# Performance work log

Hardware: AMD Instinct MI355X
Metric: run time of the kernel (lower is better)

The kernel has to match this reference:

```python
import jax, jax.numpy as jnp
import numpy as np

N_SRC = 100000
N_DST = 100000
N_EDGES = 1000000
D = 64


def setup_inputs() -> dict:
    key = jax.random.key(0)
    k1, k2, k3 = jax.random.split(key, 3)
    src_emb = jax.random.normal(k1, (N_SRC, D), dtype=jnp.float32)
    edge_src = jax.random.randint(k2, (N_EDGES,), 0, N_SRC, dtype=jnp.int64)
    edge_dst = jax.random.randint(k3, (N_EDGES,), 0, N_DST, dtype=jnp.int64)
    return {"src_emb": src_emb, "edge_src": edge_src, "edge_dst": edge_dst, "num_dst": N_DST}


def reference(src_emb, edge_src, edge_dst, num_dst):
    # copy_u: gather source features onto edges; sum: scatter-add to dst nodes.
    messages = src_emb[edge_src]  # [E, D]
    dst_emb = jax.ops.segment_sum(messages, edge_dst, num_segments=num_dst)  # [N_dst, D]
    return dst_emb
```

## Files before the change

kernel.cpp:

```cpp
#include <hip/hip_runtime.h>


#define DPB 256
#define BIN_SHIFT 8
#define EPB 4096

__device__ __forceinline__ unsigned short f2bf(float f) {
    unsigned u = __float_as_uint(f);
    unsigned r = u + 0x7FFFu + ((u >> 16) & 1u);
    return (unsigned short)(r >> 16);
}
__device__ __forceinline__ unsigned pack2(float lo, float hi) {
    return (unsigned)f2bf(lo) | ((unsigned)f2bf(hi) << 16);
}

__global__ void convert_bf16_kernel(const float4* __restrict__ src4,
                                    uint4* __restrict__ srcb, long n8) {
    long t = (long)blockIdx.x * blockDim.x + threadIdx.x;
    if (t >= n8) return;
    float4 a = src4[t * 2];
    float4 b = src4[t * 2 + 1];
    uint4 o;
    o.x = pack2(a.x, a.y);
    o.y = pack2(a.z, a.w);
    o.z = pack2(b.x, b.y);
    o.w = pack2(b.z, b.w);
    srcb[t] = o;
}

__global__ void bin_hist_kernel(const int* __restrict__ edst,
                                int* __restrict__ binCounts,
                                int nbins, int n) {
    __shared__ int lc[1024];
    int t = threadIdx.x;
    for (int k = t; k < nbins; k += blockDim.x) lc[k] = 0;
    __syncthreads();

    int i0 = blockIdx.x * EPB + t * 8;
    if (i0 + 7 < n) {
        int4 d0 = *reinterpret_cast<const int4*>(edst + i0);
        int4 d1 = *reinterpret_cast<const int4*>(edst + i0 + 4);
        atomicAdd(&lc[d0.x >> BIN_SHIFT], 1);
        atomicAdd(&lc[d0.y >> BIN_SHIFT], 1);
        atomicAdd(&lc[d0.z >> BIN_SHIFT], 1);
        atomicAdd(&lc[d0.w >> BIN_SHIFT], 1);
        atomicAdd(&lc[d1.x >> BIN_SHIFT], 1);
        atomicAdd(&lc[d1.y >> BIN_SHIFT], 1);
        atomicAdd(&lc[d1.z >> BIN_SHIFT], 1);
        atomicAdd(&lc[d1.w >> BIN_SHIFT], 1);
    } else {
        for (int k = 0; k < 8; ++k) {
            int i = i0 + k;
            if (i < n) atomicAdd(&lc[edst[i] >> BIN_SHIFT], 1);
        }
    }
    __syncthreads();
    for (int k = t; k < nbins; k += blockDim.x) {
        int c = lc[k];
        if (c > 0) atomicAdd(&binCounts[k], c);
    }
}

__global__ void bin_scan_kernel(int* __restrict__ binOff,
                                int* __restrict__ cursor,
                                int nbins) {
    __shared__ int lds[1024];
    int t = threadIdx.x;
    int v = (t < nbins) ? binOff[t] : 0;
    lds[t] = v;
    __syncthreads();
    for (int off = 1; off < 1024; off <<= 1) {
        int u = (t >= off) ? lds[t - off] : 0;
        __syncthreads();
        lds[t] += u;
        __syncthreads();
    }
    if (t < nbins) {
        int base = lds[t] - v;
        binOff[t] = base;
        cursor[t] = base;
    }
    if (t == 1023) binOff[nbins] = lds[t];
}

__global__ void bin_scatter_kernel(const int* __restrict__ esrc,
                                   const int* __restrict__ edst,
                                   int* __restrict__ cursor,
                                   int* __restrict__ packed,
                                   int nbins, int n) {
    __shared__ int lc[1024];
    __shared__ int lbase[1024];
    __shared__ int lrank[1024];
    int t = threadIdx.x;
    for (int k = t; k < nbins; k += blockDim.x) { lc[k] = 0; lrank[k] = 0; }
    __syncthreads();

    int i0 = blockIdx.x * EPB + t * 8;
    bool fast = (i0 + 7 < n);

    if (fast) {
        int4 d0 = *reinterpret_cast<const int4*>(edst + i0);
        int4 d1 = *reinterpret_cast<const int4*>(edst + i0 + 4);
        atomicAdd(&lc[d0.x >> BIN_SHIFT], 1);
        atomicAdd(&lc[d0.y >> BIN_SHIFT], 1);
        atomicAdd(&lc[d0.z >> BIN_SHIFT], 1);
        atomicAdd(&lc[d0.w >> BIN_SHIFT], 1);
        atomicAdd(&lc[d1.x >> BIN_SHIFT], 1);
        atomicAdd(&lc[d1.y >> BIN_SHIFT], 1);
        atomicAdd(&lc[d1.z >> BIN_SHIFT], 1);
        atomicAdd(&lc[d1.w >> BIN_SHIFT], 1);
    } else {
        for (int k = 0; k < 8; ++k) {
            int i = i0 + k;
            if (i < n) atomicAdd(&lc[edst[i] >> BIN_SHIFT], 1);
        }
    }
    __syncthreads();

    for (int k = t; k < nbins; k += blockDim.x) {
        int c = lc[k];
        if (c > 0) lbase[k] = atomicAdd(&cursor[k], c);
    }
    __syncthreads();

    if (fast) {
        int4 s0 = *reinterpret_cast<const int4*>(esrc + i0);
        int4 s1 = *reinterpret_cast<const int4*>(esrc + i0 + 4);
        int4 d0 = *reinterpret_cast<const int4*>(edst + i0);
        int4 d1 = *reinterpret_cast<const int4*>(edst + i0 + 4);
        { int k = d0.x >> BIN_SHIFT, r = atomicAdd(&lrank[k], 1);
          packed[lbase[k] + r] = ((d0.x & (DPB - 1)) << 20) | s0.x; }
        { int k = d0.y >> BIN_SHIFT, r = atomicAdd(&lrank[k], 1);
          packed[lbase[k] + r] = ((d0.y & (DPB - 1)) << 20) | s0.y; }
        { int k = d0.z >> BIN_SHIFT, r = atomicAdd(&lrank[k], 1);
          packed[lbase[k] + r] = ((d0.z & (DPB - 1)) << 20) | s0.z; }
        { int k = d0.w >> BIN_SHIFT, r = atomicAdd(&lrank[k], 1);
          packed[lbase[k] + r] = ((d0.w & (DPB - 1)) << 20) | s0.w; }
        { int k = d1.x >> BIN_SHIFT, r = atomicAdd(&lrank[k], 1);
          packed[lbase[k] + r] = ((d1.x & (DPB - 1)) << 20) | s1.x; }
        { int k = d1.y >> BIN_SHIFT, r = atomicAdd(&lrank[k], 1);
          packed[lbase[k] + r] = ((d1.y & (DPB - 1)) << 20) | s1.y; }
        { int k = d1.z >> BIN_SHIFT, r = atomicAdd(&lrank[k], 1);
          packed[lbase[k] + r] = ((d1.z & (DPB - 1)) << 20) | s1.z; }
        { int k = d1.w >> BIN_SHIFT, r = atomicAdd(&lrank[k], 1);
          packed[lbase[k] + r] = ((d1.w & (DPB - 1)) << 20) | s1.w; }
    } else {
        for (int kk = 0; kk < 8; ++kk) {
            int i = i0 + kk;
            if (i < n) {
                int d = edst[i];
                int k = d >> BIN_SHIFT;
                int r = atomicAdd(&lrank[k], 1);
                packed[lbase[k] + r] = ((d & (DPB - 1)) << 20) | esrc[i];
            }
        }
    }
}

__global__ void bin_sort_kernel(const int* __restrict__ packed,
                                const int* __restrict__ binOff,
                                int* __restrict__ sorted_src,
                                int* __restrict__ offsets,
                                int nbins, int n_dst, int n_edges) {
    __shared__ int cnt[DPB];
    __shared__ int base[DPB];
    int t = threadIdx.x;
    int b = blockIdx.x;
    int start = binOff[b];
    int end = binOff[b + 1];

    cnt[t] = 0;
    __syncthreads();
    for (int j = start + t; j < end; j += DPB) {
        atomicAdd(&cnt[(packed[j] >> 20) & (DPB - 1)], 1);
    }
    __syncthreads();
    int v = cnt[t];
    base[t] = v;
    __syncthreads();
    for (int o = 1; o < DPB; o <<= 1) {
        int u = (t >= o) ? base[t - o] : 0;
        __syncthreads();
        base[t] += u;
        __syncthreads();
    }
    int my_excl = base[t] - v;
    __syncthreads();
    base[t] = my_excl;
    cnt[t] = 0;
    int g = (b << BIN_SHIFT) + t;
    if (g < n_dst) offsets[g] = start + my_excl;
    if (b == nbins - 1 && t == 0) offsets[n_dst] = n_edges;
    __syncthreads();
    for (int j = start + t; j < end; j += DPB) {
        int p = packed[j];
        int dl = (p >> 20) & (DPB - 1);
        int r = atomicAdd(&cnt[dl], 1);
        sorted_src[start + base[dl] + r] = p & 0xFFFFF;
    }
}

__global__ void accum_abs_bf16(const uint4* __restrict__ srcb,
                               const int* __restrict__ offsets,
                               const int* __restrict__ sorted_src,
                               float4* __restrict__ out4, int n_dst) {
    int node = blockIdx.x * (blockDim.x >> 6) + (threadIdx.x >> 6);
    if (node >= n_dst) return;
    int lane = threadIdx.x & 63;
    int g = lane >> 3;
    int q = lane & 7;

    int start = offsets[node];
    int end = offsets[node + 1];

    float a0 = 0.f, a1 = 0.f, a2 = 0.f, a3 = 0.f;
    float a4 = 0.f, a5 = 0.f, a6 = 0.f, a7 = 0.f;

    for (int j = start + g; j < end; j += 8) {
        int s = sorted_src[j];
        uint4 v = srcb[(size_t)s * 8 + q];
        a0 += __uint_as_float(v.x << 16);
        a1 += __uint_as_float(v.x & 0xFFFF0000u);
        a2 += __uint_as_float(v.y << 16);
        a3 += __uint_as_float(v.y & 0xFFFF0000u);
        a4 += __uint_as_float(v.z << 16);
        a5 += __uint_as_float(v.z & 0xFFFF0000u);
        a6 += __uint_as_float(v.w << 16);
        a7 += __uint_as_float(v.w & 0xFFFF0000u);
    }

#pragma unroll
    for (int off = 8; off < 64; off <<= 1) {
        a0 += __shfl_xor(a0, off);
        a1 += __shfl_xor(a1, off);
        a2 += __shfl_xor(a2, off);
        a3 += __shfl_xor(a3, off);
        a4 += __shfl_xor(a4, off);
        a5 += __shfl_xor(a5, off);
        a6 += __shfl_xor(a6, off);
        a7 += __shfl_xor(a7, off);
    }
    if (g == 0) {
        size_t o = (size_t)node * 16 + q * 2;
        out4[o]     = make_float4(a0, a1, a2, a3);
        out4[o + 1] = make_float4(a4, a5, a6, a7);
    }
}


__global__ void fused_bucket_convert(const float4* __restrict__ src4,
                                     uint4* __restrict__ srcb, long n8,
                                     const int* __restrict__ esrc,
                                     const int* __restrict__ edst,
                                     int* __restrict__ cnt,
                                     int* __restrict__ bucket, int cap,
                                     int2* __restrict__ spill,
                                     int* __restrict__ spill_cnt, int spill_max,
                                     int n_edges) {
    int i = blockIdx.x * blockDim.x + threadIdx.x;

    int s = 0, r = 0, d = 0;
    bool have_edge = (i < n_edges);
    if (have_edge) {
        d = edst[i];
        s = esrc[i];
        r = atomicAdd(&cnt[d], 1);
    }

    long nthreads = (long)gridDim.x * blockDim.x;
    for (long t = i; t < n8; t += nthreads) {
        float4 a = src4[t * 2];
        float4 b = src4[t * 2 + 1];
        uint4 o;
        o.x = pack2(a.x, a.y);
        o.y = pack2(a.z, a.w);
        o.z = pack2(b.x, b.y);
        o.w = pack2(b.z, b.w);
        srcb[t] = o;
    }

    if (have_edge) {
        if (r < cap) {
            bucket[(size_t)d * cap + r] = s;
        } else {
            int k = atomicAdd(spill_cnt, 1);
            if (k < spill_max) spill[k] = make_int2(s, d);
        }
    }
}

__global__ void accum_bucket_bf16(const uint4* __restrict__ srcb,
                                  const int* __restrict__ cnt,
                                  const int* __restrict__ bucket, int cap,
                                  float4* __restrict__ out4, int n_dst) {
    int node = blockIdx.x * (blockDim.x >> 6) + (threadIdx.x >> 6);
    if (node >= n_dst) return;
    int lane = threadIdx.x & 63;
    int g = lane >> 3;
    int q = lane & 7;

    int cn = cnt[node];
    cn = cn < cap ? cn : cap;
    const int* brow = bucket + (size_t)node * cap;

    float a0 = 0.f, a1 = 0.f, a2 = 0.f, a3 = 0.f;
    float a4 = 0.f, a5 = 0.f, a6 = 0.f, a7 = 0.f;

    for (int j = g; j < cn; j += 8) {
        int s = brow[j];
        uint4 v = srcb[(size_t)s * 8 + q];
        a0 += __uint_as_float(v.x << 16);
        a1 += __uint_as_float(v.x & 0xFFFF0000u);
        a2 += __uint_as_float(v.y << 16);
        a3 += __uint_as_float(v.y & 0xFFFF0000u);
        a4 += __uint_as_float(v.z << 16);
        a5 += __uint_as_float(v.z & 0xFFFF0000u);
        a6 += __uint_as_float(v.w << 16);
        a7 += __uint_as_float(v.w & 0xFFFF0000u);
    }

#pragma unroll
    for (int off = 8; off < 64; off <<= 1) {
        a0 += __shfl_xor(a0, off);
        a1 += __shfl_xor(a1, off);
        a2 += __shfl_xor(a2, off);
        a3 += __shfl_xor(a3, off);
        a4 += __shfl_xor(a4, off);
        a5 += __shfl_xor(a5, off);
        a6 += __shfl_xor(a6, off);
        a7 += __shfl_xor(a7, off);
    }
    if (g == 0) {
        size_t o = (size_t)node * 16 + q * 2;
        out4[o]     = make_float4(a0, a1, a2, a3);
        out4[o + 1] = make_float4(a4, a5, a6, a7);
    }
}

__global__ void spill_add_kernel(const float* __restrict__ src_emb,
                                 const int2* __restrict__ spill,
                                 const int* __restrict__ spill_cnt,
                                 int spill_max, float* __restrict__ out) {
    int n = *spill_cnt;
    if (n > spill_max) n = spill_max;
    long total = (long)n * 16;
    long stride = (long)gridDim.x * blockDim.x;
    for (long u = (long)blockIdx.x * blockDim.x + threadIdx.x; u < total;
         u += stride) {
        int e = (int)(u >> 4);
        int q = (int)(u & 15);
        int2 p = spill[e];
        const float* row = src_emb + (size_t)p.x * 64 + q * 4;
        float* orow = out + (size_t)p.y * 64 + q * 4;
        atomicAdd(orow + 0, row[0]);
        atomicAdd(orow + 1, row[1]);
        atomicAdd(orow + 2, row[2]);
        atomicAdd(orow + 3, row[3]);
    }
}

__global__ void atomic_scatter_kernel(const float* __restrict__ src_emb,
                                      const int* __restrict__ esrc,
                                      const int* __restrict__ edst,
                                      float* __restrict__ out, int n_edges) {
    int tid = blockIdx.x * blockDim.x + threadIdx.x;
    int e = tid >> 4;
    int q = tid & 15;
    if (e >= n_edges) return;
    int s = esrc[e];
    int d = edst[e];
    const float4* srow = reinterpret_cast<const float4*>(src_emb);
    float4 v = srow[(size_t)s * 16 + q];
    float* orow = out + (size_t)d * 64 + (size_t)q * 4;
    atomicAdd(orow + 0, v.x);
    atomicAdd(orow + 1, v.y);
    atomicAdd(orow + 2, v.z);
    atomicAdd(orow + 3, v.w);
}

extern "C" void kernel_launch(void* const* d_in, const int* in_sizes, int n_in,
                              void* d_out, int out_size, void* d_ws, size_t ws_size,
                              hipStream_t stream) {
    const float* src_emb = (const float*)d_in[0];
    const int* edge_src  = (const int*)d_in[1];
    const int* edge_dst  = (const int*)d_in[2];
    float* out = (float*)d_out;

    const int n_edges = in_sizes[1];
    const int n_src   = in_sizes[0] / 64;
    const int n_dst   = out_size / 64;

    const int B = 256;
    long n8 = (long)n_src * 8;
    size_t ws_ints = ws_size / sizeof(int);

    {
        int nbins = (n_dst + DPB - 1) >> BIN_SHIFT;
        size_t srcb_ints = (size_t)n_src * 32;
        size_t need0 = srcb_ints + (size_t)nbins + 1 + nbins +
                       (size_t)n_edges + (size_t)n_dst + 1 + (size_t)n_edges;
        if (n_dst > 0 && n_edges > 0 && n_src > 0 && n_src <= (1 << 20) &&
            nbins >= 1 && nbins <= 1024 && ws_ints >= need0) {
            uint4* srcb     = (uint4*)d_ws;
            int* binOff     = (int*)d_ws + srcb_ints;
            int* cursor     = binOff + nbins + 1;
            int* packed     = cursor + nbins;
            int* offsets    = packed + n_edges;
            int* sorted_src = offsets + n_dst + 1;

            int eblocks = (n_edges + EPB - 1) / EPB;
            int nodes_per_block = B / 64;
            int agrid = (n_dst + nodes_per_block - 1) / nodes_per_block;

            convert_bf16_kernel<<<(int)((n8 + B - 1) / B), B, 0, stream>>>(
                reinterpret_cast<const float4*>(src_emb), srcb, n8);
            hipMemsetAsync(binOff, 0, ((size_t)nbins + 1) * sizeof(int), stream);
            bin_hist_kernel<<<eblocks, 512, 0, stream>>>(edge_dst, binOff,
                                                         nbins, n_edges);
            bin_scan_kernel<<<1, 1024, 0, stream>>>(binOff, cursor, nbins);
            bin_scatter_kernel<<<eblocks, 512, 0, stream>>>(edge_src, edge_dst,
                                                            cursor, packed,
                                                            nbins, n_edges);
            bin_sort_kernel<<<nbins, DPB, 0, stream>>>(packed, binOff,
                                                       sorted_src, offsets,
                                                       nbins, n_dst, n_edges);
            accum_abs_bf16<<<agrid, B, 0, stream>>>(
                srcb, offsets, sorted_src,
                reinterpret_cast<float4*>(out), n_dst);
            return;
        }
    }

    if (n_dst > 0 && n_src > 0 && n_edges > 0) {
        size_t srcb_ints  = (size_t)n_src * 32;
        size_t cnt_ints   = ((size_t)n_dst + 1 + 1) & ~(size_t)1;
        int spill_entries = n_edges < 262144 ? n_edges : 262144;
        size_t spill_ints = 2 * (size_t)spill_entries;
        size_t fixed = srcb_ints + cnt_ints + spill_ints;
        if (ws_ints > fixed) {
            long cap_l = (long)((ws_ints - fixed) / (size_t)n_dst);
            cap_l &= ~1L;
            int cap = cap_l > 64 ? 64 : (int)cap_l;
            if (cap >= 24) {
                uint4* srcb    = (uint4*)d_ws;
                int* cnt       = (int*)d_ws + srcb_ints;
                int* spill_cnt = cnt + n_dst;
                int* bucket    = (int*)d_ws + srcb_ints + cnt_ints;
                int2* spill    = (int2*)(bucket + (size_t)n_dst * cap);

                int egrid1 = (n_edges + B - 1) / B;
                int nodes_per_block = B / 64;
                int agrid = (n_dst + nodes_per_block - 1) / nodes_per_block;

                hipMemsetAsync(cnt, 0, ((size_t)n_dst + 1) * sizeof(int), stream);
                fused_bucket_convert<<<egrid1, B, 0, stream>>>(
                    reinterpret_cast<const float4*>(src_emb), srcb, n8,
                    edge_src, edge_dst, cnt, bucket, cap,
                    spill, spill_cnt, spill_entries, n_edges);
                accum_bucket_bf16<<<agrid, B, 0, stream>>>(
                    srcb, cnt, bucket, cap,
                    reinterpret_cast<float4*>(out), n_dst);
                spill_add_kernel<<<16, B, 0, stream>>>(
                    src_emb, spill, spill_cnt, spill_entries, out);
                return;
            }
        }
    }

    hipMemsetAsync(d_out, 0, (size_t)out_size * sizeof(float), stream);
    int total = n_edges * 16;
    atomic_scatter_kernel<<<(total + 255) / 256, 256, 0, stream>>>(
        src_emb, edge_src, edge_dst, out, n_edges);
}
```

Measured before the change: 81.41 us.

## Replace histogram+scan with fixed-capacity bins, fuse convert into scatter, LDS bin sort

Adds a new first-choice path that gives each destination bin a fixed-capacity slot, so the histogram pass, the global scan and the memset are no longer needed. Edges beyond a bin's capacity go to a spill list that a small kernel adds afterwards. The bf16 conversion of the source embeddings is folded into the scatter kernel. The per-bin sort now stages entries in shared memory and sorts in place, writing separate start and end arrays instead of a dense offset array. This cuts kernel launches and passes over the edges, at the cost of padded workspace, dynamic LDS up to 64KB per block, and a spill path for skewed degree distributions.

```diff
diff --git a/kernel.cpp b/kernel.cpp
--- a/kernel.cpp
+++ b/kernel.cpp
@@ -14,80 +14,23 @@
     return (unsigned)f2bf(lo) | ((unsigned)f2bf(hi) << 16);
 }
 
-__global__ void convert_bf16_kernel(const float4* __restrict__ src4,
-                                    uint4* __restrict__ srcb, long n8) {
-    long t = (long)blockIdx.x * blockDim.x + threadIdx.x;
-    if (t >= n8) return;
-    float4 a = src4[t * 2];
-    float4 b = src4[t * 2 + 1];
-    uint4 o;
-    o.x = pack2(a.x, a.y);
-    o.y = pack2(a.z, a.w);
-    o.z = pack2(b.x, b.y);
-    o.w = pack2(b.z, b.w);
-    srcb[t] = o;
-}
-
-__global__ void bin_hist_kernel(const int* __restrict__ edst,
-                                int* __restrict__ binCounts,
-                                int nbins, int n) {
-    __shared__ int lc[1024];
-    int t = threadIdx.x;
-    for (int k = t; k < nbins; k += blockDim.x) lc[k] = 0;
-    __syncthreads();
-
-    int i0 = blockIdx.x * EPB + t * 8;
-    if (i0 + 7 < n) {
-        int4 d0 = *reinterpret_cast<const int4*>(edst + i0);
-        int4 d1 = *reinterpret_cast<const int4*>(edst + i0 + 4);
-        atomicAdd(&lc[d0.x >> BIN_SHIFT], 1);
-        atomicAdd(&lc[d0.y >> BIN_SHIFT], 1);
-        atomicAdd(&lc[d0.z >> BIN_SHIFT], 1);
-        atomicAdd(&lc[d0.w >> BIN_SHIFT], 1);
-        atomicAdd(&lc[d1.x >> BIN_SHIFT], 1);
-        atomicAdd(&lc[d1.y >> BIN_SHIFT], 1);
-        atomicAdd(&lc[d1.z >> BIN_SHIFT], 1);
-        atomicAdd(&lc[d1.w >> BIN_SHIFT], 1);
-    } else {
-        for (int k = 0; k < 8; ++k) {
-            int i = i0 + k;
-            if (i < n) atomicAdd(&lc[edst[i] >> BIN_SHIFT], 1);
-        }
-    }
-    __syncthreads();
-    for (int k = t; k < nbins; k += blockDim.x) {
-        int c = lc[k];
-        if (c > 0) atomicAdd(&binCounts[k], c);
-    }
-}
-
-__global__ void bin_scan_kernel(int* __restrict__ binOff,
-                                int* __restrict__ cursor,
-                                int nbins) {
-    __shared__ int lds[1024];
-    int t = threadIdx.x;
-    int v = (t < nbins) ? binOff[t] : 0;
-    lds[t] = v;
-    __syncthreads();
-    for (int off = 1; off < 1024; off <<= 1) {
-        int u = (t >= off) ? lds[t - off] : 0;
-        __syncthreads();
-        lds[t] += u;
-        __syncthreads();
-    }
-    if (t < nbins) {
-        int base = lds[t] - v;
-        binOff[t] = base;
-        cursor[t] = base;
-    }
-    if (t == 1023) binOff[nbins] = lds[t];
-}
-
-__global__ void bin_scatter_kernel(const int* __restrict__ esrc,
-                                   const int* __restrict__ edst,
-                                   int* __restrict__ cursor,
-                                   int* __restrict__ packed,
-                                   int nbins, int n) {
+__global__ void init_cursor_kernel(int* __restrict__ cursor,
+                                   int* __restrict__ spill_cnt,
+                                   int nbins, int cap) {
+    int b = blockIdx.x * blockDim.x + threadIdx.x;
+    if (b < nbins) cursor[b] = b * cap;
+    if (b == 0) *spill_cnt = 0;
+}
+
+__global__ void scatter_convert_kernel(const float4* __restrict__ src4,
+                                       uint4* __restrict__ srcb, long n8,
+                                       const int* __restrict__ esrc,
+                                       const int* __restrict__ edst,
+                                       int* __restrict__ cursor,
+                                       int* __restrict__ packed, int cap,
+                                       int2* __restrict__ spill,
+                                       int* __restrict__ spill_cnt,
+                                       int spill_max, int nbins, int n) {
     __shared__ int lc[1024];
     __shared__ int lbase[1024];
     __shared__ int lrank[1024];
@@ -121,6 +64,18 @@
         int c = lc[k];
         if (c > 0) lbase[k] = atomicAdd(&cursor[k], c);
     }
+
+    long nthreads = (long)gridDim.x * blockDim.x;
+    for (long u = (long)blockIdx.x * blockDim.x + t; u < n8; u += nthreads) {
+        float4 a = src4[u * 2];
+        float4 b = src4[u * 2 + 1];
+        uint4 o;
+        o.x = pack2(a.x, a.y);
+        o.y = pack2(a.z, a.w);
+        o.z = pack2(b.x, b.y);
+        o.w = pack2(b.z, b.w);
+        srcb[u] = o;
+    }
     __syncthreads();
 
     if (fast) {
@@ -128,53 +83,64 @@
         int4 s1 = *reinterpret_cast<const int4*>(esrc + i0 + 4);
         int4 d0 = *reinterpret_cast<const int4*>(edst + i0);
         int4 d1 = *reinterpret_cast<const int4*>(edst + i0 + 4);
-        { int k = d0.x >> BIN_SHIFT, r = atomicAdd(&lrank[k], 1);
-          packed[lbase[k] + r] = ((d0.x & (DPB - 1)) << 20) | s0.x; }
-        { int k = d0.y >> BIN_SHIFT, r = atomicAdd(&lrank[k], 1);
-          packed[lbase[k] + r] = ((d0.y & (DPB - 1)) << 20) | s0.y; }
-        { int k = d0.z >> BIN_SHIFT, r = atomicAdd(&lrank[k], 1);
-          packed[lbase[k] + r] = ((d0.z & (DPB - 1)) << 20) | s0.z; }
-        { int k = d0.w >> BIN_SHIFT, r = atomicAdd(&lrank[k], 1);
-          packed[lbase[k] + r] = ((d0.w & (DPB - 1)) << 20) | s0.w; }
-        { int k = d1.x >> BIN_SHIFT, r = atomicAdd(&lrank[k], 1);
-          packed[lbase[k] + r] = ((d1.x & (DPB - 1)) << 20) | s1.x; }
-        { int k = d1.y >> BIN_SHIFT, r = atomicAdd(&lrank[k], 1);
-          packed[lbase[k] + r] = ((d1.y & (DPB - 1)) << 20) | s1.y; }
-        { int k = d1.z >> BIN_SHIFT, r = atomicAdd(&lrank[k], 1);
-          packed[lbase[k] + r] = ((d1.z & (DPB - 1)) << 20) | s1.z; }
-        { int k = d1.w >> BIN_SHIFT, r = atomicAdd(&lrank[k], 1);
-          packed[lbase[k] + r] = ((d1.w & (DPB - 1)) << 20) | s1.w; }
+        int dd[8] = {d0.x, d0.y, d0.z, d0.w, d1.x, d1.y, d1.z, d1.w};
+        int ss[8] = {s0.x, s0.y, s0.z, s0.w, s1.x, s1.y, s1.z, s1.w};
+#pragma unroll
+        for (int e = 0; e < 8; ++e) {
+            int d = dd[e], s = ss[e];
+            int k = d >> BIN_SHIFT;
+            int r = atomicAdd(&lrank[k], 1);
+            int pos = lbase[k] + r;
+            if (pos < (k + 1) * cap) {
+                packed[pos] = ((d & (DPB - 1)) << 20) | s;
+            } else {
+                int sp = atomicAdd(spill_cnt, 1);
+                if (sp < spill_max) spill[sp] = make_int2(s, d);
+            }
+        }
     } else {
         for (int kk = 0; kk < 8; ++kk) {
             int i = i0 + kk;
             if (i < n) {
-                int d = edst[i];
+                int d = edst[i], s = esrc[i];
                 int k = d >> BIN_SHIFT;
                 int r = atomicAdd(&lrank[k], 1);
-                packed[lbase[k] + r] = ((d & (DPB - 1)) << 20) | esrc[i];
+                int pos = lbase[k] + r;
+                if (pos < (k + 1) * cap) {
+                    packed[pos] = ((d & (DPB - 1)) << 20) | s;
+                } else {
+                    int sp = atomicAdd(spill_cnt, 1);
+                    if (sp < spill_max) spill[sp] = make_int2(s, d);
+                }
             }
         }
     }
 }
 
-__global__ void bin_sort_kernel(const int* __restrict__ packed,
-                                const int* __restrict__ binOff,
-                                int* __restrict__ sorted_src,
-                                int* __restrict__ offsets,
-                                int nbins, int n_dst, int n_edges) {
-    __shared__ int cnt[DPB];
-    __shared__ int base[DPB];
+__global__ void bin_sort_lds_kernel(int* __restrict__ packed,
+                                    const int* __restrict__ cursor,
+                                    int* __restrict__ offsets,
+                                    int* __restrict__ ends,
+                                    int cap, int nbins, int n_dst) {
+    extern __shared__ int smem[];
+    int* buf  = smem;
+    int* cnt  = smem + cap;
+    int* base = cnt + DPB;
     int t = threadIdx.x;
     int b = blockIdx.x;
-    int start = binOff[b];
-    int end = binOff[b + 1];
-
+    int start = b * cap;
+    int count = cursor[b] - start;
+    if (count > cap) count = cap;
+    if (count < 0) count = 0;
+
+    for (int j = t; j < count; j += DPB) buf[j] = packed[start + j];
     cnt[t] = 0;
     __syncthreads();
-    for (int j = start + t; j < end; j += DPB) {
-        atomicAdd(&cnt[(packed[j] >> 20) & (DPB - 1)], 1);
-    }
-    __syncthreads();
+
+    for (int j = t; j < count; j += DPB)
+        atomicAdd(&cnt[(buf[j] >> 20) & (DPB - 1)], 1);
+    __syncthreads();
+
     int v = cnt[t];
     base[t] = v;
     __syncthreads();
@@ -184,24 +150,28 @@
         base[t] += u;
         __syncthreads();
     }
-    int my_excl = base[t] - v;
-    __syncthreads();
-    base[t] = my_excl;
+    int excl = base[t] - v;
+    __syncthreads();
+    base[t] = excl;
     cnt[t] = 0;
     int g = (b << BIN_SHIFT) + t;
-    if (g < n_dst) offsets[g] = start + my_excl;
-    if (b == nbins - 1 && t == 0) offsets[n_dst] = n_edges;
-    __syncthreads();
-    for (int j = start + t; j < end; j += DPB) {
-        int p = packed[j];
+    if (g < n_dst) {
+        offsets[g] = start + excl;
+        ends[g]    = start + excl + v;
+    }
+    __syncthreads();
+
+    for (int j = t; j < count; j += DPB) {
+        int p = buf[j];
         int dl = (p >> 20) & (DPB - 1);
         int r = atomicAdd(&cnt[dl], 1);
-        sorted_src[start + base[dl] + r] = p & 0xFFFFF;
-    }
-}
-
-__global__ void accum_abs_bf16(const uint4* __restrict__ srcb,
+        packed[start + base[dl] + r] = p & 0xFFFFF;
+    }
+}
+
+__global__ void accum_fix_bf16(const uint4* __restrict__ srcb,
                                const int* __restrict__ offsets,
+                               const int* __restrict__ ends,
                                const int* __restrict__ sorted_src,
                                float4* __restrict__ out4, int n_dst) {
     int node = blockIdx.x * (blockDim.x >> 6) + (threadIdx.x >> 6);
@@ -211,103 +181,13 @@
     int q = lane & 7;
 
     int start = offsets[node];
-    int end = offsets[node + 1];
+    int end = ends[node];
 
     float a0 = 0.f, a1 = 0.f, a2 = 0.f, a3 = 0.f;
     float a4 = 0.f, a5 = 0.f, a6 = 0.f, a7 = 0.f;
 
     for (int j = start + g; j < end; j += 8) {
         int s = sorted_src[j];
-        uint4 v = srcb[(size_t)s * 8 + q];
-        a0 += __uint_as_float(v.x << 16);
-        a1 += __uint_as_float(v.x & 0xFFFF0000u);
-        a2 += __uint_as_float(v.y << 16);
-        a3 += __uint_as_float(v.y & 0xFFFF0000u);
-        a4 += __uint_as_float(v.z << 16);
-        a5 += __uint_as_float(v.z & 0xFFFF0000u);
-        a6 += __uint_as_float(v.w << 16);
-        a7 += __uint_as_float(v.w & 0xFFFF0000u);
-    }
-
-#pragma unroll
-    for (int off = 8; off < 64; off <<= 1) {
-        a0 += __shfl_xor(a0, off);
-        a1 += __shfl_xor(a1, off);
-        a2 += __shfl_xor(a2, off);
-        a3 += __shfl_xor(a3, off);
-        a4 += __shfl_xor(a4, off);
-        a5 += __shfl_xor(a5, off);
-        a6 += __shfl_xor(a6, off);
-        a7 += __shfl_xor(a7, off);
-    }
-    if (g == 0) {
-        size_t o = (size_t)node * 16 + q * 2;
-        out4[o]     = make_float4(a0, a1, a2, a3);
-        out4[o + 1] = make_float4(a4, a5, a6, a7);
-    }
-}
-
-
-__global__ void fused_bucket_convert(const float4* __restrict__ src4,
-                                     uint4* __restrict__ srcb, long n8,
-                                     const int* __restrict__ esrc,
-                                     const int* __restrict__ edst,
-                                     int* __restrict__ cnt,
-                                     int* __restrict__ bucket, int cap,
-                                     int2* __restrict__ spill,
-                                     int* __restrict__ spill_cnt, int spill_max,
-                                     int n_edges) {
-    int i = blockIdx.x * blockDim.x + threadIdx.x;
-
-    int s = 0, r = 0, d = 0;
-    bool have_edge = (i < n_edges);
-    if (have_edge) {
-        d = edst[i];
-        s = esrc[i];
-        r = atomicAdd(&cnt[d], 1);
-    }
-
-    long nthreads = (long)gridDim.x * blockDim.x;
-    for (long t = i; t < n8; t += nthreads) {
-        float4 a = src4[t * 2];
-        float4 b = src4[t * 2 + 1];
-        uint4 o;
-        o.x = pack2(a.x, a.y);
-        o.y = pack2(a.z, a.w);
-        o.z = pack2(b.x, b.y);
-        o.w = pack2(b.z, b.w);
-        srcb[t] = o;
-    }
-
-    if (have_edge) {
-        if (r < cap) {
-            bucket[(size_t)d * cap + r] = s;
-        } else {
-            int k = atomicAdd(spill_cnt, 1);
-            if (k < spill_max) spill[k] = make_int2(s, d);
-        }
-    }
-}
-
-__global__ void accum_bucket_bf16(const uint4* __restrict__ srcb,
-                                  const int* __restrict__ cnt,
-                                  const int* __restrict__ bucket, int cap,
-                                  float4* __restrict__ out4, int n_dst) {
-    int node = blockIdx.x * (blockDim.x >> 6) + (threadIdx.x >> 6);
-    if (node >= n_dst) return;
-    int lane = threadIdx.x & 63;
-    int g = lane >> 3;
-    int q = lane & 7;
-
-    int cn = cnt[node];
-    cn = cn < cap ? cn : cap;
-    const int* brow = bucket + (size_t)node * cap;
-
-    float a0 = 0.f, a1 = 0.f, a2 = 0.f, a3 = 0.f;
-    float a4 = 0.f, a5 = 0.f, a6 = 0.f, a7 = 0.f;
-
-    for (int j = g; j < cn; j += 8) {
-        int s = brow[j];
         uint4 v = srcb[(size_t)s * 8 + q];
         a0 += __uint_as_float(v.x << 16);
         a1 += __uint_as_float(v.x & 0xFFFF0000u);
@@ -359,6 +239,220 @@
     }
 }
 
+
+__global__ void convert_bf16_kernel(const float4* __restrict__ src4,
+                                    uint4* __restrict__ srcb, long n8) {
+    long t = (long)blockIdx.x * blockDim.x + threadIdx.x;
+    if (t >= n8) return;
+    float4 a = src4[t * 2];
+    float4 b = src4[t * 2 + 1];
+    uint4 o;
+    o.x = pack2(a.x, a.y);
+    o.y = pack2(a.z, a.w);
+    o.z = pack2(b.x, b.y);
+    o.w = pack2(b.z, b.w);
+    srcb[t] = o;
+}
+
+__global__ void bin_hist_kernel(const int* __restrict__ edst,
+                                int* __restrict__ binCounts,
+                                int nbins, int n) {
+    __shared__ int lc[1024];
+    int t = threadIdx.x;
+    for (int k = t; k < nbins; k += blockDim.x) lc[k] = 0;
+    __syncthreads();
+    int i0 = blockIdx.x * EPB + t * 8;
+    if (i0 + 7 < n) {
+        int4 d0 = *reinterpret_cast<const int4*>(edst + i0);
+        int4 d1 = *reinterpret_cast<const int4*>(edst + i0 + 4);
+        atomicAdd(&lc[d0.x >> BIN_SHIFT], 1);
+        atomicAdd(&lc[d0.y >> BIN_SHIFT], 1);
+        atomicAdd(&lc[d0.z >> BIN_SHIFT], 1);
+        atomicAdd(&lc[d0.w >> BIN_SHIFT], 1);
+        atomicAdd(&lc[d1.x >> BIN_SHIFT], 1);
+        atomicAdd(&lc[d1.y >> BIN_SHIFT], 1);
+        atomicAdd(&lc[d1.z >> BIN_SHIFT], 1);
+        atomicAdd(&lc[d1.w >> BIN_SHIFT], 1);
+    } else {
+        for (int k = 0; k < 8; ++k) {
+            int i = i0 + k;
+            if (i < n) atomicAdd(&lc[edst[i] >> BIN_SHIFT], 1);
+        }
+    }
+    __syncthreads();
+    for (int k = t; k < nbins; k += blockDim.x) {
+        int c = lc[k];
+        if (c > 0) atomicAdd(&binCounts[k], c);
+    }
+}
+
+__global__ void bin_scan_kernel(int* __restrict__ binOff,
+                                int* __restrict__ cursor, int nbins) {
+    __shared__ int lds[1024];
+    int t = threadIdx.x;
+    int v = (t < nbins) ? binOff[t] : 0;
+    lds[t] = v;
+    __syncthreads();
+    for (int off = 1; off < 1024; off <<= 1) {
+        int u = (t >= off) ? lds[t - off] : 0;
+        __syncthreads();
+        lds[t] += u;
+        __syncthreads();
+    }
+    if (t < nbins) {
+        int base = lds[t] - v;
+        binOff[t] = base;
+        cursor[t] = base;
+    }
+    if (t == 1023) binOff[nbins] = lds[t];
+}
+
+__global__ void bin_scatter_kernel(const int* __restrict__ esrc,
+                                   const int* __restrict__ edst,
+                                   int* __restrict__ cursor,
+                                   int* __restrict__ packed,
+                                   int nbins, int n) {
+    __shared__ int lc[1024];
+    __shared__ int lbase[1024];
+    __shared__ int lrank[1024];
+    int t = threadIdx.x;
+    for (int k = t; k < nbins; k += blockDim.x) { lc[k] = 0; lrank[k] = 0; }
+    __syncthreads();
+    int i0 = blockIdx.x * EPB + t * 8;
+    bool fast = (i0 + 7 < n);
+    if (fast) {
+        int4 d0 = *reinterpret_cast<const int4*>(edst + i0);
+        int4 d1 = *reinterpret_cast<const int4*>(edst + i0 + 4);
+        atomicAdd(&lc[d0.x >> BIN_SHIFT], 1);
+        atomicAdd(&lc[d0.y >> BIN_SHIFT], 1);
+        atomicAdd(&lc[d0.z >> BIN_SHIFT], 1);
+        atomicAdd(&lc[d0.w >> BIN_SHIFT], 1);
+        atomicAdd(&lc[d1.x >> BIN_SHIFT], 1);
+        atomicAdd(&lc[d1.y >> BIN_SHIFT], 1);
+        atomicAdd(&lc[d1.z >> BIN_SHIFT], 1);
+        atomicAdd(&lc[d1.w >> BIN_SHIFT], 1);
+    } else {
+        for (int k = 0; k < 8; ++k) {
+            int i = i0 + k;
+            if (i < n) atomicAdd(&lc[edst[i] >> BIN_SHIFT], 1);
+        }
+    }
+    __syncthreads();
+    for (int k = t; k < nbins; k += blockDim.x) {
+        int c = lc[k];
+        if (c > 0) lbase[k] = atomicAdd(&cursor[k], c);
+    }
+    __syncthreads();
+    if (fast) {
+        int4 s0 = *reinterpret_cast<const int4*>(esrc + i0);
+        int4 s1 = *reinterpret_cast<const int4*>(esrc + i0 + 4);
+        int4 d0 = *reinterpret_cast<const int4*>(edst + i0);
+        int4 d1 = *reinterpret_cast<const int4*>(edst + i0 + 4);
+        int dd[8] = {d0.x, d0.y, d0.z, d0.w, d1.x, d1.y, d1.z, d1.w};
+        int ss[8] = {s0.x, s0.y, s0.z, s0.w, s1.x, s1.y, s1.z, s1.w};
+#pragma unroll
+        for (int e = 0; e < 8; ++e) {
+            int k = dd[e] >> BIN_SHIFT;
+            int r = atomicAdd(&lrank[k], 1);
+            packed[lbase[k] + r] = ((dd[e] & (DPB - 1)) << 20) | ss[e];
+        }
+    } else {
+        for (int kk = 0; kk < 8; ++kk) {
+            int i = i0 + kk;
+            if (i < n) {
+                int d = edst[i];
+                int k = d >> BIN_SHIFT;
+                int r = atomicAdd(&lrank[k], 1);
+                packed[lbase[k] + r] = ((d & (DPB - 1)) << 20) | esrc[i];
+            }
+        }
+    }
+}
+
+__global__ void bin_sort_kernel(const int* __restrict__ packed,
+                                const int* __restrict__ binOff,
+                                int* __restrict__ sorted_src,
+                                int* __restrict__ offsets,
+                                int nbins, int n_dst, int n_edges) {
+    __shared__ int cnt[DPB];
+    __shared__ int base[DPB];
+    int t = threadIdx.x;
+    int b = blockIdx.x;
+    int start = binOff[b];
+    int end = binOff[b + 1];
+    cnt[t] = 0;
+    __syncthreads();
+    for (int j = start + t; j < end; j += DPB)
+        atomicAdd(&cnt[(packed[j] >> 20) & (DPB - 1)], 1);
+    __syncthreads();
+    int v = cnt[t];
+    base[t] = v;
+    __syncthreads();
+    for (int o = 1; o < DPB; o <<= 1) {
+        int u = (t >= o) ? base[t - o] : 0;
+        __syncthreads();
+        base[t] += u;
+        __syncthreads();
+    }
+    int my_excl = base[t] - v;
+    __syncthreads();
+    base[t] = my_excl;
+    cnt[t] = 0;
+    int g = (b << BIN_SHIFT) + t;
+    if (g < n_dst) offsets[g] = start + my_excl;
+    if (b == nbins - 1 && t == 0) offsets[n_dst] = n_edges;
+    __syncthreads();
+    for (int j = start + t; j < end; j += DPB) {
+        int p = packed[j];
+        int dl = (p >> 20) & (DPB - 1);
+        int r = atomicAdd(&cnt[dl], 1);
+        sorted_src[start + base[dl] + r] = p & 0xFFFFF;
+    }
+}
+
+__global__ void accum_abs_bf16(const uint4* __restrict__ srcb,
+                               const int* __restrict__ offsets,
+                               const int* __restrict__ sorted_src,
+                               float4* __restrict__ out4, int n_dst) {
+    int node = blockIdx.x * (blockDim.x >> 6) + (threadIdx.x >> 6);
+    if (node >= n_dst) return;
+    int lane = threadIdx.x & 63;
+    int g = lane >> 3;
+    int q = lane & 7;
+    int start = offsets[node];
+    int end = offsets[node + 1];
+    float a0 = 0.f, a1 = 0.f, a2 = 0.f, a3 = 0.f;
+    float a4 = 0.f, a5 = 0.f, a6 = 0.f, a7 = 0.f;
+    for (int j = start + g; j < end; j += 8) {
+        int s = sorted_src[j];
+        uint4 v = srcb[(size_t)s * 8 + q];
+        a0 += __uint_as_float(v.x << 16);
+        a1 += __uint_as_float(v.x & 0xFFFF0000u);
+        a2 += __uint_as_float(v.y << 16);
+        a3 += __uint_as_float(v.y & 0xFFFF0000u);
+        a4 += __uint_as_float(v.z << 16);
+        a5 += __uint_as_float(v.z & 0xFFFF0000u);
+        a6 += __uint_as_float(v.w << 16);
+        a7 += __uint_as_float(v.w & 0xFFFF0000u);
+    }
+#pragma unroll
+    for (int off = 8; off < 64; off <<= 1) {
+        a0 += __shfl_xor(a0, off);
+        a1 += __shfl_xor(a1, off);
+        a2 += __shfl_xor(a2, off);
+        a3 += __shfl_xor(a3, off);
+        a4 += __shfl_xor(a4, off);
+        a5 += __shfl_xor(a5, off);
+        a6 += __shfl_xor(a6, off);
+        a7 += __shfl_xor(a7, off);
+    }
+    if (g == 0) {
+        size_t o = (size_t)node * 16 + q * 2;
+        out4[o]     = make_float4(a0, a1, a2, a3);
+        out4[o + 1] = make_float4(a4, a5, a6, a7);
+    }
+}
+
 __global__ void atomic_scatter_kernel(const float* __restrict__ src_emb,
                                       const int* __restrict__ esrc,
                                       const int* __restrict__ edst,
@@ -393,24 +487,62 @@
     const int B = 256;
     long n8 = (long)n_src * 8;
     size_t ws_ints = ws_size / sizeof(int);
+    int nbins = (n_dst + DPB - 1) >> BIN_SHIFT;
+    int eblocks = (n_edges + EPB - 1) / EPB;
+    int nodes_per_block = B / 64;
+    int agrid = (n_dst + nodes_per_block - 1) / nodes_per_block;
+
+    if (n_dst > 0 && n_edges > 0 && n_src > 0 && n_src <= (1 << 20) &&
+        nbins >= 1 && nbins <= 1024) {
+        size_t srcb_ints = (size_t)n_src * 32;
+        int spill_max = 65536;
+        size_t fixed = srcb_ints + nbins + 1 + 2 * (size_t)n_dst +
+                       2 * (size_t)spill_max;
+        if (ws_ints > fixed) {
+            long cap_l = (long)((ws_ints - fixed) / (size_t)nbins);
+            int cap = cap_l > 8192 ? 8192 : (int)cap_l;
+            long avg = (long)n_edges / nbins;
+            if (cap >= 3072 && (long)cap >= avg + 512 &&
+                (size_t)(cap + 2 * DPB) * 4 <= 64 * 1024) {
+                uint4* srcb    = (uint4*)d_ws;
+                int* cursor    = (int*)d_ws + srcb_ints;
+                int* spill_cnt = cursor + nbins;
+                int* offsets   = spill_cnt + 1;
+                int* ends      = offsets + n_dst;
+                int2* spill    = (int2*)(ends + n_dst);
+                int* packed    = (int*)(spill + spill_max);
+
+                init_cursor_kernel<<<(nbins + B - 1) / B, B, 0, stream>>>(
+                    cursor, spill_cnt, nbins, cap);
+                scatter_convert_kernel<<<eblocks, 512, 0, stream>>>(
+                    reinterpret_cast<const float4*>(src_emb), srcb, n8,
+                    edge_src, edge_dst, cursor, packed, cap,
+                    spill, spill_cnt, spill_max, nbins, n_edges);
+                size_t shmem = (size_t)(cap + 2 * DPB) * sizeof(int);
+                bin_sort_lds_kernel<<<nbins, DPB, shmem, stream>>>(
+                    packed, cursor, offsets, ends, cap, nbins, n_dst);
+                accum_fix_bf16<<<agrid, B, 0, stream>>>(
+                    srcb, offsets, ends, packed,
+                    reinterpret_cast<float4*>(out), n_dst);
+                spill_add_kernel<<<16, B, 0, stream>>>(
+                    src_emb, spill, spill_cnt, spill_max, out);
+                return;
+            }
+        }
+    }
 
     {
-        int nbins = (n_dst + DPB - 1) >> BIN_SHIFT;
         size_t srcb_ints = (size_t)n_src * 32;
-        size_t need0 = srcb_ints + (size_t)nbins + 1 + nbins +
+        size_t need1 = srcb_ints + (size_t)nbins + 1 + nbins +
                        (size_t)n_edges + (size_t)n_dst + 1 + (size_t)n_edges;
         if (n_dst > 0 && n_edges > 0 && n_src > 0 && n_src <= (1 << 20) &&
-            nbins >= 1 && nbins <= 1024 && ws_ints >= need0) {
+            nbins >= 1 && nbins <= 1024 && ws_ints >= need1) {
             uint4* srcb     = (uint4*)d_ws;
             int* binOff     = (int*)d_ws + srcb_ints;
             int* cursor     = binOff + nbins + 1;
             int* packed     = cursor + nbins;
             int* offsets    = packed + n_edges;
             int* sorted_src = offsets + n_dst + 1;
-
-            int eblocks = (n_edges + EPB - 1) / EPB;
-            int nodes_per_block = B / 64;
-            int agrid = (n_dst + nodes_per_block - 1) / nodes_per_block;
 
             convert_bf16_kernel<<<(int)((n8 + B - 1) / B), B, 0, stream>>>(
                 reinterpret_cast<const float4*>(src_emb), srcb, n8);
@@ -431,42 +563,6 @@
         }
     }
 
-    if (n_dst > 0 && n_src > 0 && n_edges > 0) {
-        size_t srcb_ints  = (size_t)n_src * 32;
-        size_t cnt_ints   = ((size_t)n_dst + 1 + 1) & ~(size_t)1;
-        int spill_entries = n_edges < 262144 ? n_edges : 262144;
-        size_t spill_ints = 2 * (size_t)spill_entries;
-        size_t fixed = srcb_ints + cnt_ints + spill_ints;
-        if (ws_ints > fixed) {
-            long cap_l = (long)((ws_ints - fixed) / (size_t)n_dst);
-            cap_l &= ~1L;
-            int cap = cap_l > 64 ? 64 : (int)cap_l;
-            if (cap >= 24) {
-                uint4* srcb    = (uint4*)d_ws;
-                int* cnt       = (int*)d_ws + srcb_ints;
-                int* spill_cnt = cnt + n_dst;
-                int* bucket    = (int*)d_ws + srcb_ints + cnt_ints;
-                int2* spill    = (int2*)(bucket + (size_t)n_dst * cap);
-
-                int egrid1 = (n_edges + B - 1) / B;
-                int nodes_per_block = B / 64;
-                int agrid = (n_dst + nodes_per_block - 1) / nodes_per_block;
-
-                hipMemsetAsync(cnt, 0, ((size_t)n_dst + 1) * sizeof(int), stream);
-                fused_bucket_convert<<<egrid1, B, 0, stream>>>(
-                    reinterpret_cast<const float4*>(src_emb), srcb, n8,
-                    edge_src, edge_dst, cnt, bucket, cap,
-                    spill, spill_cnt, spill_entries, n_edges);
-                accum_bucket_bf16<<<agrid, B, 0, stream>>>(
-                    srcb, cnt, bucket, cap,
-                    reinterpret_cast<float4*>(out), n_dst);
-                spill_add_kernel<<<16, B, 0, stream>>>(
-                    src_emb, spill, spill_cnt, spill_entries, out);
-                return;
-            }
-        }
-    }
-
     hipMemsetAsync(d_out, 0, (size_t)out_size * sizeof(float), stream);
     int total = n_edges * 16;
     atomic_scatter_kernel<<<(total + 255) / 256, 256, 0, stream>>>(
```

New measurement: 71.53 us. 1.14x faster.
